# Kernel optimization log

Measured on AMD Instinct MI355X. Metric: run time of the kernel, lower is better.

Reference implementation:

```python
import jax, jax.numpy as jnp
import numpy as np

B, N, D = 8, 2048, 1024

def setup_inputs() -> dict:
    key = jax.random.key(0)
    k1, k2, k3, k4 = jax.random.split(key, 4)
    q = jax.random.normal(k1, (B, N, D), dtype=jnp.float32)
    k = jax.random.normal(k2, (B, N, D), dtype=jnp.float32)
    v = jax.random.uniform(k3, (B, N, N), dtype=jnp.float32)
    # nn.Linear default init (kaiming-uniform-ish); scale is irrelevant for correctness
    bound = 1.0 / np.sqrt(D)
    W1 = jax.random.uniform(k4, (D, D), dtype=jnp.float32, minval=-bound, maxval=bound)
    b1 = jnp.zeros((D,), dtype=jnp.float32)
    return {"q": q, "k": k, "v": v, "W1": W1, "b1": b1}

def adj_normalization(adj):
    # D^{-1/2} A D^{-1/2} with rowsum clamped at 1; expressed as O(N^2)
    # broadcast scaling instead of the original's two diagonal bmms.
    rowsum = jnp.maximum(adj.sum(-1), 1.0)          # [B, N]
    d_inv_sqrt = rowsum ** -0.5                      # [B, N]
    return d_inv_sqrt[:, :, None] * adj * d_inv_sqrt[:, None, :]

def reference(q, k, v, W1, b1):
    # ff_layers == 1: q_out = linear1(q) (dropout is identity in eval);
    # k is unused because _fc returns (q_out, q_out).
    q_out = jnp.einsum('bnd,ed->bne', q, W1) + b1    # [B, N, D]
    attn = jnp.einsum('bnd,bmd->bnm', q_out, q_out)  # [B, N, N]
    # comb_mode == 2 (learn_n_norm): symmetric normalization of attn; v unused.
    output = adj_normalization(attn)
    return (output, attn)
```

## Files before the change

kernel.cpp:

```cpp
#include <hip/hip_runtime.h>

#define B_ 8
#define N_ 2048
#define D_ 1024

using u16 = unsigned short;
typedef __attribute__((ext_vector_type(8))) short short8;
typedef __attribute__((ext_vector_type(4))) float f32x4;
typedef __attribute__((ext_vector_type(4))) float float4v;
typedef __attribute__((ext_vector_type(4))) int int4v;

static __device__ __forceinline__ float bf2f(u16 h) {
  return __uint_as_float(((unsigned)h) << 16);
}
static __device__ __forceinline__ u16 f2bf(float f) {
  unsigned u = __float_as_uint(f);
  u += 0x7FFFu + ((u >> 16) & 1u);
  return (u16)(u >> 16);
}

static __device__ __forceinline__ void gload16(const void* g, void* l) {
  __builtin_amdgcn_global_load_lds((const __attribute__((address_space(1))) void*)g,
                                   (__attribute__((address_space(3))) void*)l, 16, 0, 0);
}

static __device__ __forceinline__ void stage_slab(u16* __restrict__ L,
                                                  const u16* __restrict__ g,
                                                  int slab, int kof, int w) {
  gload16(g + (size_t)(slab * 64) * 1024 + kof, L + slab * 4096 + w * 512);
}


template<int S1, int S2, int VM>
__device__ __forceinline__ void tile_body(u16* __restrict__ cur, u16* __restrict__ nxt,
                                          const u16* __restrict__ gA, const u16* __restrict__ gB,
                                          int kn1, int kn2,
                                          int w, int wr, int wc, int lane15, int ck0,
                                          f32x4 (&acc)[8][4])
{
  const u16* Ar = cur + (wr * 128 + lane15) * 64;
  const u16* Br = cur + 16384 + (wc * 64 + lane15) * 64;
  const int ck1 = ck0 ^ 32;
  short8 a[4], bk0[4], bk1[4];

  if constexpr (VM == 2) asm volatile("s_waitcnt vmcnt(2)" ::: "memory");
  else                   asm volatile("s_waitcnt vmcnt(0)" ::: "memory");
  __builtin_amdgcn_s_barrier();

  #pragma unroll
  for (int m = 0; m < 4; ++m) a[m] = *(const short8*)(Ar + m * 1024 + ck0);
  #pragma unroll
  for (int n = 0; n < 4; ++n) bk0[n] = *(const short8*)(Br + n * 1024 + ck0);
  if constexpr (S1) { stage_slab(nxt, gA, 1, kn1, w); stage_slab(nxt, gA, 3, kn1, w); }
  __builtin_amdgcn_s_barrier();
  __builtin_amdgcn_s_setprio(1);
  #pragma unroll
  for (int m = 0; m < 4; ++m)
    #pragma unroll
    for (int n = 0; n < 4; ++n)
      acc[m][n] = __builtin_amdgcn_mfma_f32_16x16x32_bf16(a[m], bk0[n], acc[m][n], 0, 0, 0);
  __builtin_amdgcn_s_setprio(0);
  __builtin_amdgcn_s_barrier();

  #pragma unroll
  for (int m = 0; m < 4; ++m) a[m] = *(const short8*)(Ar + m * 1024 + ck1);
  #pragma unroll
  for (int n = 0; n < 4; ++n) bk1[n] = *(const short8*)(Br + n * 1024 + ck1);
  if constexpr (S1) { stage_slab(nxt + 16384, gB, 0, kn1, w); stage_slab(nxt + 16384, gB, 1, kn1, w); }
  __builtin_amdgcn_s_barrier();
  __builtin_amdgcn_s_setprio(1);
  #pragma unroll
  for (int m = 0; m < 4; ++m)
    #pragma unroll
    for (int n = 0; n < 4; ++n)
      acc[m][n] = __builtin_amdgcn_mfma_f32_16x16x32_bf16(a[m], bk1[n], acc[m][n], 0, 0, 0);
  __builtin_amdgcn_s_setprio(0);
  __builtin_amdgcn_s_barrier();

  #pragma unroll
  for (int m = 0; m < 4; ++m) a[m] = *(const short8*)(Ar + (m + 4) * 1024 + ck0);
  if constexpr (S1) { stage_slab(nxt + 16384, gB, 2, kn1, w); stage_slab(nxt + 16384, gB, 3, kn1, w); }
  __builtin_amdgcn_s_barrier();
  __builtin_amdgcn_s_setprio(1);
  #pragma unroll
  for (int m = 0; m < 4; ++m)
    #pragma unroll
    for (int n = 0; n < 4; ++n)
      acc[m + 4][n] = __builtin_amdgcn_mfma_f32_16x16x32_bf16(a[m], bk0[n], acc[m + 4][n], 0, 0, 0);
  __builtin_amdgcn_s_setprio(0);
  __builtin_amdgcn_s_barrier();

  #pragma unroll
  for (int m = 0; m < 4; ++m) a[m] = *(const short8*)(Ar + (m + 4) * 1024 + ck1);
  if constexpr (S2) { stage_slab(cur, gA, 0, kn2, w); stage_slab(cur, gA, 2, kn2, w); }
  __builtin_amdgcn_s_barrier();
  __builtin_amdgcn_s_setprio(1);
  #pragma unroll
  for (int m = 0; m < 4; ++m)
    #pragma unroll
    for (int n = 0; n < 4; ++n)
      acc[m + 4][n] = __builtin_amdgcn_mfma_f32_16x16x32_bf16(a[m], bk1[n], acc[m + 4][n], 0, 0, 0);
  __builtin_amdgcn_s_setprio(0);
  __builtin_amdgcn_s_barrier();
}

template<int MODE>
__global__ __launch_bounds__(512, 2)
void gemm8p(const u16* __restrict__ Abase, const u16* __restrict__ Bbase,
            const float* __restrict__ aux,
            void* __restrict__ C0, float* __restrict__ C1)
{
  __shared__ u16 lds[2][32768];
  const int tid = threadIdx.x;
  const int w = tid >> 6, l = tid & 63;

  int tm0, tn0, z = 0;
  if (MODE == 0) {
    const int bid = blockIdx.x;
    const int s = (bid & 7) * 32 + (bid >> 3);
    tm0 = (s >> 2) << 8;
    tn0 = (s & 3) << 8;
  } else {
    const int bid = blockIdx.x;
    const int s = (bid & 7) * 64 + (bid >> 3);
    z  = s >> 6;
    tm0 = ((s >> 3) & 7) << 8;
    tn0 = (s & 7) << 8;
  }
  const u16* A  = Abase + (MODE ? (size_t)z * N_ * D_ : 0);
  const u16* Bm = (MODE ? A : Bbase);

  const int sc = (((l & 7) ^ (l >> 3)) << 4) >> 1;
  const int sr = w * 8 + (l >> 3);
  const u16* gA = A  + (size_t)(tm0 + sr) * 1024 + sc;
  const u16* gB = Bm + (size_t)(tn0 + sr) * 1024 + sc;

  const int lane15 = l & 15, lhi = l >> 4;
  const int ck0 = ((lhi << 4) ^ ((l & 7) << 4)) >> 1;
  const int wr = w >> 2, wc = w & 3;

  f32x4 acc[8][4];
  #pragma unroll
  for (int m = 0; m < 8; ++m)
    #pragma unroll
    for (int n = 0; n < 4; ++n)
      acc[m][n] = (f32x4){0.f, 0.f, 0.f, 0.f};

  u16* cur = &lds[0][0];
  u16* nxt = &lds[1][0];

  #pragma unroll
  for (int s4 = 0; s4 < 4; ++s4) stage_slab(cur, gA, s4, 0, w);
  #pragma unroll
  for (int s4 = 0; s4 < 4; ++s4) stage_slab(cur + 16384, gB, s4, 0, w);
  stage_slab(nxt, gA, 0, 64, w);
  stage_slab(nxt, gA, 2, 64, w);

  for (int t = 0; t < 14; ++t) {
    tile_body<1, 1, 2>(cur, nxt, gA, gB, (t + 1) * 64, (t + 2) * 64,
                       w, wr, wc, lane15, ck0, acc);
    u16* tmp = cur; cur = nxt; nxt = tmp;
  }
  tile_body<1, 0, 2>(cur, nxt, gA, gB, 15 * 64, 0, w, wr, wc, lane15, ck0, acc);
  { u16* tmp = cur; cur = nxt; nxt = tmp; }
  tile_body<0, 0, 0>(cur, nxt, gA, gB, 0, 0, w, wr, wc, lane15, ck0, acc);
  asm volatile("s_waitcnt vmcnt(0)" ::: "memory");

  const int rbase = tm0 + wr * 128 + lhi * 4;
  const int cbase = tn0 + wc * 64 + lane15;

  if (MODE == 0) {
    u16* C = (u16*)C0;
    #pragma unroll
    for (int m = 0; m < 8; ++m)
      #pragma unroll
      for (int n = 0; n < 4; ++n) {
        const int col = cbase + n * 16;
        const float bv = aux[col];
        #pragma unroll
        for (int j = 0; j < 4; ++j)
          C[(size_t)(rbase + m * 16 + j) * 1024 + col] = f2bf(acc[m][n][j] + bv);
      }
  } else {
    float* Cattn = (float*)C0 + (size_t)z * N_ * N_;
    float* Cout  = C1 + (size_t)z * N_ * N_;
    const float* dv = aux + z * N_;
    float di[8][4];
    #pragma unroll
    for (int m = 0; m < 8; ++m)
      #pragma unroll
      for (int j = 0; j < 4; ++j)
        di[m][j] = dv[rbase + m * 16 + j];
    #pragma unroll
    for (int m = 0; m < 8; ++m)
      #pragma unroll
      for (int n = 0; n < 4; ++n) {
        const int col = cbase + n * 16;
        const float dj = dv[col];
        #pragma unroll
        for (int j = 0; j < 4; ++j) {
          const size_t off = (size_t)(rbase + m * 16 + j) * N_ + col;
          const float a = acc[m][n][j];
          Cattn[off] = a;
          Cout[off]  = a * di[m][j] * dj;
        }
      }
  }
}

__global__ void cvt_q_qsum(const float* __restrict__ q, u16* __restrict__ qbf,
                           float* __restrict__ qsum) {
  const int wi = blockIdx.x * 256 + threadIdx.x;
  const int d0 = (wi & 127) * 8;
  const int rc = (wi >> 7) & 127;
  const int b  = wi >> 14;
  const size_t base = ((size_t)b * N_ + rc * 16) * D_ + d0;
  float s[8];
  #pragma unroll
  for (int k = 0; k < 8; ++k) s[k] = 0.f;
  #pragma unroll 4
  for (int r = 0; r < 16; ++r) {
    const float4v* p = (const float4v*)(q + base + (size_t)r * D_);
    float4v x = p[0], y = p[1];
    union { u16 h[8]; int4v v; } o;
    o.h[0] = f2bf(x.x); o.h[1] = f2bf(x.y); o.h[2] = f2bf(x.z); o.h[3] = f2bf(x.w);
    o.h[4] = f2bf(y.x); o.h[5] = f2bf(y.y); o.h[6] = f2bf(y.z); o.h[7] = f2bf(y.w);
    *(int4v*)(qbf + base + (size_t)r * D_) = o.v;
    s[0] += x.x; s[1] += x.y; s[2] += x.z; s[3] += x.w;
    s[4] += y.x; s[5] += y.y; s[6] += y.z; s[7] += y.w;
  }
  float* qs = qsum + b * D_ + d0;
  #pragma unroll
  for (int k = 0; k < 8; ++k) atomicAdd(qs + k, s[k]);
}

__global__ void cvt_f32_to_bf16(const float* __restrict__ in, u16* __restrict__ out, int n8) {
  const int stride = gridDim.x * blockDim.x;
  for (int i = blockIdx.x * blockDim.x + threadIdx.x; i < n8; i += stride) {
    const float4v* p = (const float4v*)in + (size_t)i * 2;
    float4v a = p[0], b = p[1];
    union { u16 h[8]; int4v v; } r;
    r.h[0] = f2bf(a.x); r.h[1] = f2bf(a.y); r.h[2] = f2bf(a.z); r.h[3] = f2bf(a.w);
    r.h[4] = f2bf(b.x); r.h[5] = f2bf(b.y); r.h[6] = f2bf(b.z); r.h[7] = f2bf(b.w);
    ((int4v*)out)[i] = r.v;
  }
}

__global__ void s_kernel(const float* __restrict__ qsum, const float* __restrict__ W1,
                         const float* __restrict__ b1, float* __restrict__ s) {
  const int idx = blockIdx.x * 256 + threadIdx.x;
  const int b = idx >> 10, e = idx & (D_ - 1);
  const int d0 = blockIdx.y * 64;
  const float4v* wp = (const float4v*)(W1 + (size_t)e * D_ + d0);
  const float4v* qp = (const float4v*)(qsum + b * D_ + d0);
  float acc = 0.f;
  #pragma unroll 4
  for (int t = 0; t < 16; ++t) {
    float4v wv = wp[t], qv = qp[t];
    acc += wv.x * qv.x + wv.y * qv.y + wv.z * qv.z + wv.w * qv.w;
  }
  if (blockIdx.y == 0) acc += (float)N_ * b1[e];
  atomicAdd(&s[b * D_ + e], acc);
}

__global__ void t_kernel(const float* __restrict__ W1, const float* __restrict__ s,
                         float* __restrict__ tv) {
  const int idx = blockIdx.x * 256 + threadIdx.x;
  const int b = idx >> 10, d = idx & (D_ - 1);
  const int e0 = blockIdx.y * 64;
  const float* wp = W1 + (size_t)e0 * D_ + d;
  const float* sp = s + b * D_ + e0;
  float acc = 0.f;
  #pragma unroll 8
  for (int e = 0; e < 64; ++e) acc += wp[(size_t)e * D_] * sp[e];
  atomicAdd(&tv[b * D_ + d], acc);
}

__global__ void c_kernel(const float* __restrict__ b1, const float* __restrict__ s,
                         float* __restrict__ c) {
  const int b = blockIdx.x;
  const int tid = threadIdx.x;
  float acc = 0.f;
  #pragma unroll
  for (int t = 0; t < 4; ++t) {
    const int e = tid + t * 256;
    acc += b1[e] * s[b * D_ + e];
  }
  __shared__ float red[4];
  #pragma unroll
  for (int off = 32; off; off >>= 1) acc += __shfl_down(acc, off);
  if ((tid & 63) == 0) red[tid >> 6] = acc;
  __syncthreads();
  if (tid == 0) c[b] = red[0] + red[1] + red[2] + red[3];
}

__global__ void rowdinv_kernel(const float* __restrict__ q, const float* __restrict__ tv,
                               const float* __restrict__ c, float* __restrict__ dinv) {
  const int row  = blockIdx.x * 4 + (threadIdx.x >> 6);
  const int lane = threadIdx.x & 63;
  const int b    = row >> 11;
  const float4v* p  = (const float4v*)(q + (size_t)row * D_);
  const float4v* tp = (const float4v*)(tv + b * D_);
  float acc = 0.f;
  #pragma unroll
  for (int it = 0; it < 4; ++it) {
    float4v qv = p[it * 64 + lane];
    float4v tw = tp[it * 64 + lane];
    acc += qv.x * tw.x + qv.y * tw.y + qv.z * tw.z + qv.w * tw.w;
  }
  #pragma unroll
  for (int off = 32; off; off >>= 1) acc += __shfl_down(acc, off);
  if (lane == 0) dinv[row] = rsqrtf(fmaxf(acc + c[b], 1.0f));
}

extern "C" void kernel_launch(void* const* d_in, const int* in_sizes, int n_in,
                              void* d_out, int out_size, void* d_ws, size_t ws_size,
                              hipStream_t stream) {
  const float* q  = (const float*)d_in[0];
  const float* W1 = (const float*)d_in[3];
  const float* b1 = (const float*)d_in[4];

  float* out  = (float*)d_out;
  float* attn = out + (size_t)B_ * N_ * N_;

  char* ws = (char*)d_ws;
  u16*   qbf  = (u16*)ws;
  u16*   qout = (u16*)(ws + (size_t)33554432);
  u16*   w1bf = (u16*)(ws + (size_t)67108864);
  float* qsum = (float*)(ws + (size_t)69206016);
  float* s    = (float*)(ws + (size_t)69238784);
  float* tv   = (float*)(ws + (size_t)69271552);
  float* c    = (float*)(ws + (size_t)69304320);
  float* dinv = (float*)(ws + (size_t)69304576);

  hipMemsetAsync(qsum, 0, 3 * B_ * D_ * sizeof(float) + 256, stream);

  cvt_q_qsum<<<512, 256, 0, stream>>>(q, qbf, qsum);
  cvt_f32_to_bf16<<<512, 256, 0, stream>>>(W1, w1bf, D_ * D_ / 8);

  gemm8p<0><<<256, 512, 0, stream>>>(qbf, w1bf, b1, qout, nullptr);

  s_kernel<<<dim3(B_ * D_ / 256, 16), 256, 0, stream>>>(qsum, W1, b1, s);
  t_kernel<<<dim3(B_ * D_ / 256, 16), 256, 0, stream>>>(W1, s, tv);
  c_kernel<<<B_, 256, 0, stream>>>(b1, s, c);
  rowdinv_kernel<<<(B_ * N_) / 4, 256, 0, stream>>>(q, tv, c, dinv);

  gemm8p<1><<<512, 512, 0, stream>>>(qout, nullptr, dinv, attn, out);
}
```

Measured before the change: 217.1 us.

## Switch GEMMs to 32x32x16 MFMA and fuse conversion and stats kernels

The GEMM inner loop now uses 32x32x16 bf16 MFMA tiles with f32x16 accumulators instead of 16x16x32 tiles, which halves the number of MFMA issues and LDS fragment loads per k-step. The epilogues are rewritten for the 32x32 output layout. Separately, the q and W1 bf16 conversion kernels are merged into one launch, and the s/t/c statistic kernels are merged into a single 8-block kernel without atomics. The fused stats kernel runs on only 8 blocks with a serial 1024-length loop per thread, so it may become a latency bottleneck, and the new epilogue store pattern differs from the old one.

```diff
diff --git a/kernel.cpp b/kernel.cpp
--- a/kernel.cpp
+++ b/kernel.cpp
@@ -6,13 +6,10 @@
 
 using u16 = unsigned short;
 typedef __attribute__((ext_vector_type(8))) short short8;
-typedef __attribute__((ext_vector_type(4))) float f32x4;
+typedef __attribute__((ext_vector_type(16))) float f32x16;
 typedef __attribute__((ext_vector_type(4))) float float4v;
 typedef __attribute__((ext_vector_type(4))) int int4v;
 
-static __device__ __forceinline__ float bf2f(u16 h) {
-  return __uint_as_float(((unsigned)h) << 16);
-}
 static __device__ __forceinline__ u16 f2bf(float f) {
   unsigned u = __float_as_uint(f);
   u += 0x7FFFu + ((u >> 16) & 1u);
@@ -30,78 +27,95 @@
   gload16(g + (size_t)(slab * 64) * 1024 + kof, L + slab * 4096 + w * 512);
 }
 
+#define MF32(a, b, c) __builtin_amdgcn_mfma_f32_32x32x16_bf16(a, b, c, 0, 0, 0)
+
 
 template<int S1, int S2, int VM>
 __device__ __forceinline__ void tile_body(u16* __restrict__ cur, u16* __restrict__ nxt,
                                           const u16* __restrict__ gA, const u16* __restrict__ gB,
                                           int kn1, int kn2,
-                                          int w, int wr, int wc, int lane15, int ck0,
-                                          f32x4 (&acc)[8][4])
+                                          int w, int wr, int wc, int l,
+                                          f32x16 (&acc)[4][2])
 {
-  const u16* Ar = cur + (wr * 128 + lane15) * 64;
-  const u16* Br = cur + 16384 + (wc * 64 + lane15) * 64;
-  const int ck1 = ck0 ^ 32;
-  short8 a[4], bk0[4], bk1[4];
+  const int l31 = l & 31, lhi = l >> 5, l7 = l & 7;
+  const u16* Ap = cur + (wr * 128) * 64;
+  const u16* Bp = cur + 16384 + (wc * 64) * 64;
+
+#define AFR(rt, ks) (*(const short8*)(Ap + ((rt) * 32 + l31) * 64 + ((((ks) * 2 + lhi) ^ l7) * 8)))
+#define BFR(ct, ks) (*(const short8*)(Bp + ((ct) * 32 + l31) * 64 + ((((ks) * 2 + lhi) ^ l7) * 8)))
+
+  short8 a2[2][2];
+  short8 b[2][4];
 
   if constexpr (VM == 2) asm volatile("s_waitcnt vmcnt(2)" ::: "memory");
   else                   asm volatile("s_waitcnt vmcnt(0)" ::: "memory");
   __builtin_amdgcn_s_barrier();
 
   #pragma unroll
-  for (int m = 0; m < 4; ++m) a[m] = *(const short8*)(Ar + m * 1024 + ck0);
-  #pragma unroll
-  for (int n = 0; n < 4; ++n) bk0[n] = *(const short8*)(Br + n * 1024 + ck0);
+  for (int r = 0; r < 2; ++r) { a2[r][0] = AFR(r, 0); a2[r][1] = AFR(r, 1); }
+  #pragma unroll
+  for (int cc = 0; cc < 2; ++cc) { b[cc][0] = BFR(cc, 0); b[cc][1] = BFR(cc, 1); }
   if constexpr (S1) { stage_slab(nxt, gA, 1, kn1, w); stage_slab(nxt, gA, 3, kn1, w); }
   __builtin_amdgcn_s_barrier();
   __builtin_amdgcn_s_setprio(1);
   #pragma unroll
-  for (int m = 0; m < 4; ++m)
-    #pragma unroll
-    for (int n = 0; n < 4; ++n)
-      acc[m][n] = __builtin_amdgcn_mfma_f32_16x16x32_bf16(a[m], bk0[n], acc[m][n], 0, 0, 0);
+  for (int r = 0; r < 2; ++r)
+    #pragma unroll
+    for (int cc = 0; cc < 2; ++cc)
+      #pragma unroll
+      for (int ks = 0; ks < 2; ++ks)
+        acc[r][cc] = MF32(a2[r][ks], b[cc][ks], acc[r][cc]);
   __builtin_amdgcn_s_setprio(0);
   __builtin_amdgcn_s_barrier();
 
   #pragma unroll
-  for (int m = 0; m < 4; ++m) a[m] = *(const short8*)(Ar + m * 1024 + ck1);
-  #pragma unroll
-  for (int n = 0; n < 4; ++n) bk1[n] = *(const short8*)(Br + n * 1024 + ck1);
+  for (int r = 0; r < 2; ++r) { a2[r][0] = AFR(r, 2); a2[r][1] = AFR(r, 3); }
+  #pragma unroll
+  for (int cc = 0; cc < 2; ++cc) { b[cc][2] = BFR(cc, 2); b[cc][3] = BFR(cc, 3); }
   if constexpr (S1) { stage_slab(nxt + 16384, gB, 0, kn1, w); stage_slab(nxt + 16384, gB, 1, kn1, w); }
   __builtin_amdgcn_s_barrier();
   __builtin_amdgcn_s_setprio(1);
   #pragma unroll
-  for (int m = 0; m < 4; ++m)
-    #pragma unroll
-    for (int n = 0; n < 4; ++n)
-      acc[m][n] = __builtin_amdgcn_mfma_f32_16x16x32_bf16(a[m], bk1[n], acc[m][n], 0, 0, 0);
+  for (int r = 0; r < 2; ++r)
+    #pragma unroll
+    for (int cc = 0; cc < 2; ++cc)
+      #pragma unroll
+      for (int ks = 0; ks < 2; ++ks)
+        acc[r][cc] = MF32(a2[r][ks], b[cc][2 + ks], acc[r][cc]);
   __builtin_amdgcn_s_setprio(0);
   __builtin_amdgcn_s_barrier();
 
   #pragma unroll
-  for (int m = 0; m < 4; ++m) a[m] = *(const short8*)(Ar + (m + 4) * 1024 + ck0);
+  for (int r = 0; r < 2; ++r) { a2[r][0] = AFR(r + 2, 0); a2[r][1] = AFR(r + 2, 1); }
   if constexpr (S1) { stage_slab(nxt + 16384, gB, 2, kn1, w); stage_slab(nxt + 16384, gB, 3, kn1, w); }
   __builtin_amdgcn_s_barrier();
   __builtin_amdgcn_s_setprio(1);
   #pragma unroll
-  for (int m = 0; m < 4; ++m)
-    #pragma unroll
-    for (int n = 0; n < 4; ++n)
-      acc[m + 4][n] = __builtin_amdgcn_mfma_f32_16x16x32_bf16(a[m], bk0[n], acc[m + 4][n], 0, 0, 0);
+  for (int r = 0; r < 2; ++r)
+    #pragma unroll
+    for (int cc = 0; cc < 2; ++cc)
+      #pragma unroll
+      for (int ks = 0; ks < 2; ++ks)
+        acc[r + 2][cc] = MF32(a2[r][ks], b[cc][ks], acc[r + 2][cc]);
   __builtin_amdgcn_s_setprio(0);
   __builtin_amdgcn_s_barrier();
 
   #pragma unroll
-  for (int m = 0; m < 4; ++m) a[m] = *(const short8*)(Ar + (m + 4) * 1024 + ck1);
+  for (int r = 0; r < 2; ++r) { a2[r][0] = AFR(r + 2, 2); a2[r][1] = AFR(r + 2, 3); }
   if constexpr (S2) { stage_slab(cur, gA, 0, kn2, w); stage_slab(cur, gA, 2, kn2, w); }
   __builtin_amdgcn_s_barrier();
   __builtin_amdgcn_s_setprio(1);
   #pragma unroll
-  for (int m = 0; m < 4; ++m)
-    #pragma unroll
-    for (int n = 0; n < 4; ++n)
-      acc[m + 4][n] = __builtin_amdgcn_mfma_f32_16x16x32_bf16(a[m], bk1[n], acc[m + 4][n], 0, 0, 0);
+  for (int r = 0; r < 2; ++r)
+    #pragma unroll
+    for (int cc = 0; cc < 2; ++cc)
+      #pragma unroll
+      for (int ks = 0; ks < 2; ++ks)
+        acc[r + 2][cc] = MF32(a2[r][ks], b[cc][2 + ks], acc[r + 2][cc]);
   __builtin_amdgcn_s_setprio(0);
   __builtin_amdgcn_s_barrier();
+#undef AFR
+#undef BFR
 }
 
 template<int MODE>
@@ -130,21 +144,19 @@
   const u16* A  = Abase + (MODE ? (size_t)z * N_ * D_ : 0);
   const u16* Bm = (MODE ? A : Bbase);
 
-  const int sc = (((l & 7) ^ (l >> 3)) << 4) >> 1;
+  const int sc = ((l & 7) ^ (l >> 3)) * 8;
   const int sr = w * 8 + (l >> 3);
   const u16* gA = A  + (size_t)(tm0 + sr) * 1024 + sc;
   const u16* gB = Bm + (size_t)(tn0 + sr) * 1024 + sc;
 
-  const int lane15 = l & 15, lhi = l >> 4;
-  const int ck0 = ((lhi << 4) ^ ((l & 7) << 4)) >> 1;
   const int wr = w >> 2, wc = w & 3;
 
-  f32x4 acc[8][4];
-  #pragma unroll
-  for (int m = 0; m < 8; ++m)
-    #pragma unroll
-    for (int n = 0; n < 4; ++n)
-      acc[m][n] = (f32x4){0.f, 0.f, 0.f, 0.f};
+  f32x16 acc[4][2];
+  #pragma unroll
+  for (int m = 0; m < 4; ++m)
+    #pragma unroll
+    for (int n = 0; n < 2; ++n)
+      acc[m][n] = (f32x16)(0.f);
 
   u16* cur = &lds[0][0];
   u16* nxt = &lds[1][0];
@@ -158,140 +170,130 @@
 
   for (int t = 0; t < 14; ++t) {
     tile_body<1, 1, 2>(cur, nxt, gA, gB, (t + 1) * 64, (t + 2) * 64,
-                       w, wr, wc, lane15, ck0, acc);
+                       w, wr, wc, l, acc);
     u16* tmp = cur; cur = nxt; nxt = tmp;
   }
-  tile_body<1, 0, 2>(cur, nxt, gA, gB, 15 * 64, 0, w, wr, wc, lane15, ck0, acc);
+  tile_body<1, 0, 2>(cur, nxt, gA, gB, 15 * 64, 0, w, wr, wc, l, acc);
   { u16* tmp = cur; cur = nxt; nxt = tmp; }
-  tile_body<0, 0, 0>(cur, nxt, gA, gB, 0, 0, w, wr, wc, lane15, ck0, acc);
+  tile_body<0, 0, 0>(cur, nxt, gA, gB, 0, 0, w, wr, wc, l, acc);
   asm volatile("s_waitcnt vmcnt(0)" ::: "memory");
 
+  const int l31 = l & 31, lhi = l >> 5;
   const int rbase = tm0 + wr * 128 + lhi * 4;
-  const int cbase = tn0 + wc * 64 + lane15;
+  const int cb    = tn0 + wc * 64 + l31;
 
   if (MODE == 0) {
     u16* C = (u16*)C0;
-    #pragma unroll
-    for (int m = 0; m < 8; ++m)
-      #pragma unroll
-      for (int n = 0; n < 4; ++n) {
-        const int col = cbase + n * 16;
-        const float bv = aux[col];
+    const float bv0 = aux[cb], bv1 = aux[cb + 32];
+    #pragma unroll
+    for (int rt = 0; rt < 4; ++rt)
+      #pragma unroll
+      for (int g = 0; g < 4; ++g)
         #pragma unroll
-        for (int j = 0; j < 4; ++j)
-          C[(size_t)(rbase + m * 16 + j) * 1024 + col] = f2bf(acc[m][n][j] + bv);
-      }
+        for (int jj = 0; jj < 4; ++jj) {
+          const int row = rbase + rt * 32 + g * 8 + jj;
+          C[(size_t)row * 1024 + cb]      = f2bf(acc[rt][0][g * 4 + jj] + bv0);
+          C[(size_t)row * 1024 + cb + 32] = f2bf(acc[rt][1][g * 4 + jj] + bv1);
+        }
   } else {
     float* Cattn = (float*)C0 + (size_t)z * N_ * N_;
     float* Cout  = C1 + (size_t)z * N_ * N_;
     const float* dv = aux + z * N_;
-    float di[8][4];
-    #pragma unroll
-    for (int m = 0; m < 8; ++m)
-      #pragma unroll
-      for (int j = 0; j < 4; ++j)
-        di[m][j] = dv[rbase + m * 16 + j];
-    #pragma unroll
-    for (int m = 0; m < 8; ++m)
-      #pragma unroll
-      for (int n = 0; n < 4; ++n) {
-        const int col = cbase + n * 16;
-        const float dj = dv[col];
+    const float dj0 = dv[cb], dj1 = dv[cb + 32];
+    #pragma unroll
+    for (int rt = 0; rt < 4; ++rt)
+      #pragma unroll
+      for (int g = 0; g < 4; ++g)
         #pragma unroll
-        for (int j = 0; j < 4; ++j) {
-          const size_t off = (size_t)(rbase + m * 16 + j) * N_ + col;
-          const float a = acc[m][n][j];
-          Cattn[off] = a;
-          Cout[off]  = a * di[m][j] * dj;
+        for (int jj = 0; jj < 4; ++jj) {
+          const int row = rbase + rt * 32 + g * 8 + jj;
+          const float di = dv[row];
+          const float a0 = acc[rt][0][g * 4 + jj];
+          const float a1 = acc[rt][1][g * 4 + jj];
+          const size_t off = (size_t)row * N_ + cb;
+          Cattn[off]      = a0;
+          Cout[off]       = a0 * di * dj0;
+          Cattn[off + 32] = a1;
+          Cout[off + 32]  = a1 * di * dj1;
         }
-      }
-  }
-}
-
-__global__ void cvt_q_qsum(const float* __restrict__ q, u16* __restrict__ qbf,
-                           float* __restrict__ qsum) {
-  const int wi = blockIdx.x * 256 + threadIdx.x;
-  const int d0 = (wi & 127) * 8;
-  const int rc = (wi >> 7) & 127;
-  const int b  = wi >> 14;
-  const size_t base = ((size_t)b * N_ + rc * 16) * D_ + d0;
-  float s[8];
-  #pragma unroll
-  for (int k = 0; k < 8; ++k) s[k] = 0.f;
-  #pragma unroll 4
-  for (int r = 0; r < 16; ++r) {
-    const float4v* p = (const float4v*)(q + base + (size_t)r * D_);
-    float4v x = p[0], y = p[1];
-    union { u16 h[8]; int4v v; } o;
-    o.h[0] = f2bf(x.x); o.h[1] = f2bf(x.y); o.h[2] = f2bf(x.z); o.h[3] = f2bf(x.w);
-    o.h[4] = f2bf(y.x); o.h[5] = f2bf(y.y); o.h[6] = f2bf(y.z); o.h[7] = f2bf(y.w);
-    *(int4v*)(qbf + base + (size_t)r * D_) = o.v;
-    s[0] += x.x; s[1] += x.y; s[2] += x.z; s[3] += x.w;
-    s[4] += y.x; s[5] += y.y; s[6] += y.z; s[7] += y.w;
-  }
-  float* qs = qsum + b * D_ + d0;
-  #pragma unroll
-  for (int k = 0; k < 8; ++k) atomicAdd(qs + k, s[k]);
-}
-
-__global__ void cvt_f32_to_bf16(const float* __restrict__ in, u16* __restrict__ out, int n8) {
-  const int stride = gridDim.x * blockDim.x;
-  for (int i = blockIdx.x * blockDim.x + threadIdx.x; i < n8; i += stride) {
-    const float4v* p = (const float4v*)in + (size_t)i * 2;
+  }
+}
+
+__global__ void cvt_fused(const float* __restrict__ q, u16* __restrict__ qbf,
+                          float* __restrict__ qsum,
+                          const float* __restrict__ W1, u16* __restrict__ w1bf) {
+  if (blockIdx.x < 512) {
+    const int wi = blockIdx.x * 256 + threadIdx.x;
+    const int d0 = (wi & 127) * 8;
+    const int rc = (wi >> 7) & 127;
+    const int b  = wi >> 14;
+    const size_t base = ((size_t)b * N_ + rc * 16) * D_ + d0;
+    float s[8];
+    #pragma unroll
+    for (int k = 0; k < 8; ++k) s[k] = 0.f;
+    #pragma unroll 4
+    for (int r = 0; r < 16; ++r) {
+      const float4v* p = (const float4v*)(q + base + (size_t)r * D_);
+      float4v x = p[0], y = p[1];
+      union { u16 h[8]; int4v v; } o;
+      o.h[0] = f2bf(x.x); o.h[1] = f2bf(x.y); o.h[2] = f2bf(x.z); o.h[3] = f2bf(x.w);
+      o.h[4] = f2bf(y.x); o.h[5] = f2bf(y.y); o.h[6] = f2bf(y.z); o.h[7] = f2bf(y.w);
+      *(int4v*)(qbf + base + (size_t)r * D_) = o.v;
+      s[0] += x.x; s[1] += x.y; s[2] += x.z; s[3] += x.w;
+      s[4] += y.x; s[5] += y.y; s[6] += y.z; s[7] += y.w;
+    }
+    float* qs = qsum + b * D_ + d0;
+    #pragma unroll
+    for (int k = 0; k < 8; ++k) atomicAdd(qs + k, s[k]);
+  } else {
+    const int i = (blockIdx.x - 512) * 256 + threadIdx.x;
+    const float4v* p = (const float4v*)W1 + (size_t)i * 2;
     float4v a = p[0], b = p[1];
     union { u16 h[8]; int4v v; } r;
     r.h[0] = f2bf(a.x); r.h[1] = f2bf(a.y); r.h[2] = f2bf(a.z); r.h[3] = f2bf(a.w);
     r.h[4] = f2bf(b.x); r.h[5] = f2bf(b.y); r.h[6] = f2bf(b.z); r.h[7] = f2bf(b.w);
-    ((int4v*)out)[i] = r.v;
-  }
-}
-
-__global__ void s_kernel(const float* __restrict__ qsum, const float* __restrict__ W1,
-                         const float* __restrict__ b1, float* __restrict__ s) {
-  const int idx = blockIdx.x * 256 + threadIdx.x;
-  const int b = idx >> 10, e = idx & (D_ - 1);
-  const int d0 = blockIdx.y * 64;
-  const float4v* wp = (const float4v*)(W1 + (size_t)e * D_ + d0);
-  const float4v* qp = (const float4v*)(qsum + b * D_ + d0);
+    ((int4v*)w1bf)[i] = r.v;
+  }
+}
+
+__global__ __launch_bounds__(1024)
+void fused_stats(const float* __restrict__ qsum, const float* __restrict__ W1,
+                 const float* __restrict__ b1,
+                 float* __restrict__ tv, float* __restrict__ c_out) {
+  __shared__ float s_sh[1024];
+  __shared__ float red[16];
+  const int b = blockIdx.x;
+  const int e = threadIdx.x;
+
+  const float4v* wp = (const float4v*)(W1 + (size_t)e * D_);
+  const float4v* qp = (const float4v*)(qsum + b * D_);
   float acc = 0.f;
-  #pragma unroll 4
-  for (int t = 0; t < 16; ++t) {
+  #pragma unroll 8
+  for (int t = 0; t < 256; ++t) {
     float4v wv = wp[t], qv = qp[t];
     acc += wv.x * qv.x + wv.y * qv.y + wv.z * qv.z + wv.w * qv.w;
   }
-  if (blockIdx.y == 0) acc += (float)N_ * b1[e];
-  atomicAdd(&s[b * D_ + e], acc);
-}
-
-__global__ void t_kernel(const float* __restrict__ W1, const float* __restrict__ s,
-                         float* __restrict__ tv) {
-  const int idx = blockIdx.x * 256 + threadIdx.x;
-  const int b = idx >> 10, d = idx & (D_ - 1);
-  const int e0 = blockIdx.y * 64;
-  const float* wp = W1 + (size_t)e0 * D_ + d;
-  const float* sp = s + b * D_ + e0;
-  float acc = 0.f;
+  const float se = acc + (float)N_ * b1[e];
+  s_sh[e] = se;
+
+  float cp = b1[e] * se;
+  #pragma unroll
+  for (int off = 32; off; off >>= 1) cp += __shfl_down(cp, off);
+  if ((e & 63) == 0) red[e >> 6] = cp;
+  __syncthreads();
+
+  float tacc = 0.f;
   #pragma unroll 8
-  for (int e = 0; e < 64; ++e) acc += wp[(size_t)e * D_] * sp[e];
-  atomicAdd(&tv[b * D_ + d], acc);
-}
-
-__global__ void c_kernel(const float* __restrict__ b1, const float* __restrict__ s,
-                         float* __restrict__ c) {
-  const int b = blockIdx.x;
-  const int tid = threadIdx.x;
-  float acc = 0.f;
-  #pragma unroll
-  for (int t = 0; t < 4; ++t) {
-    const int e = tid + t * 256;
-    acc += b1[e] * s[b * D_ + e];
-  }
-  __shared__ float red[4];
-  #pragma unroll
-  for (int off = 32; off; off >>= 1) acc += __shfl_down(acc, off);
-  if ((tid & 63) == 0) red[tid >> 6] = acc;
-  __syncthreads();
-  if (tid == 0) c[b] = red[0] + red[1] + red[2] + red[3];
+  for (int e2 = 0; e2 < 1024; ++e2)
+    tacc += W1[(size_t)e2 * D_ + e] * s_sh[e2];
+  tv[b * D_ + e] = tacc;
+
+  if (e == 0) {
+    float cc = 0.f;
+    #pragma unroll
+    for (int i = 0; i < 16; ++i) cc += red[i];
+    c_out[b] = cc;
+  }
 }
 
 __global__ void rowdinv_kernel(const float* __restrict__ q, const float* __restrict__ tv,
@@ -328,21 +330,17 @@
   u16*   qout = (u16*)(ws + (size_t)33554432);
   u16*   w1bf = (u16*)(ws + (size_t)67108864);
   float* qsum = (float*)(ws + (size_t)69206016);
-  float* s    = (float*)(ws + (size_t)69238784);
   float* tv   = (float*)(ws + (size_t)69271552);
   float* c    = (float*)(ws + (size_t)69304320);
   float* dinv = (float*)(ws + (size_t)69304576);
 
-  hipMemsetAsync(qsum, 0, 3 * B_ * D_ * sizeof(float) + 256, stream);
-
-  cvt_q_qsum<<<512, 256, 0, stream>>>(q, qbf, qsum);
-  cvt_f32_to_bf16<<<512, 256, 0, stream>>>(W1, w1bf, D_ * D_ / 8);
+  hipMemsetAsync(qsum, 0, B_ * D_ * sizeof(float), stream);
+
+  cvt_fused<<<1024, 256, 0, stream>>>(q, qbf, qsum, W1, w1bf);
 
   gemm8p<0><<<256, 512, 0, stream>>>(qbf, w1bf, b1, qout, nullptr);
 
-  s_kernel<<<dim3(B_ * D_ / 256, 16), 256, 0, stream>>>(qsum, W1, b1, s);
-  t_kernel<<<dim3(B_ * D_ / 256, 16), 256, 0, stream>>>(W1, s, tv);
-  c_kernel<<<B_, 256, 0, stream>>>(b1, s, c);
+  fused_stats<<<8, 1024, 0, stream>>>(qsum, W1, b1, tv, c);
   rowdinv_kernel<<<(B_ * N_) / 4, 256, 0, stream>>>(q, tv, c, dinv);
 
   gemm8p<1><<<512, 512, 0, stream>>>(qout, nullptr, dinv, attn, out);
```

After: 365.4 us. 68.3% more time.
